# Kernel optimization log

Hardware: AMD Instinct MI355X
Metric: run time of the kernel (lower is better)

The kernel has to match this reference:

```python
import jax, jax.numpy as jnp
import numpy as np

B, L, DIM, H = 2, 2048, 2048, 16
D = DIM // H
EPS = 1e-6
CAP = 50.0
SCALE = D ** -0.5


def _rms_norm(x, w):
    # x: [B,H,L,D], normalize over last dim
    scale = jax.lax.rsqrt(jnp.maximum(jnp.mean(x * x, axis=-1, keepdims=True), EPS))
    return w * x * scale


def _rotate_half(x):
    x1, x2 = jnp.split(x, 2, axis=-1)
    return jnp.concatenate([-x2, x1], axis=-1)


def setup_inputs() -> dict:
    key = jax.random.key(0)
    ks = jax.random.split(key, 6)
    x = jax.random.normal(ks[0], (B, L, DIM), dtype=jnp.float32)
    w_qkv = jax.random.normal(ks[1], (3 * DIM, DIM), dtype=jnp.float32) * (DIM ** -0.5)
    w_out = jax.random.normal(ks[2], (DIM, DIM), dtype=jnp.float32) * (DIM ** -0.5)
    q_norm_w = jnp.ones((D,), dtype=jnp.float32)
    k_norm_w = jnp.ones((D,), dtype=jnp.float32)
    # rope tables [L, D]
    inv_freq = 1.0 / (10000.0 ** (np.arange(0, D, 2, dtype=np.float32) / D))
    t = np.arange(L, dtype=np.float32)
    freqs = np.outer(t, inv_freq)  # [L, D/2]
    emb = np.concatenate([freqs, freqs], axis=-1)  # [L, D]
    cos = jnp.asarray(np.cos(emb), dtype=jnp.float32)
    sin = jnp.asarray(np.sin(emb), dtype=jnp.float32)
    # additive causal mask [1,1,L,L]
    causal = np.triu(np.full((L, L), -1e9, dtype=np.float32), k=1)
    mask = jnp.asarray(causal)[None, None]
    return {"x": x, "w_qkv": w_qkv, "w_out": w_out, "q_norm_w": q_norm_w,
            "k_norm_w": k_norm_w, "cos": cos, "sin": sin, "mask": mask}


def reference(x, w_qkv, w_out, q_norm_w, k_norm_w, cos, sin, mask):
    b, l, _ = x.shape
    qkv = jnp.einsum('bld,ed->ble', x, w_qkv).reshape(b, l, 3, H, D)
    q, k, v = [jnp.transpose(qkv[:, :, i], (0, 2, 1, 3)) for i in range(3)]  # [B,H,L,D]
    q = _rms_norm(q, q_norm_w)
    k = _rms_norm(k, k_norm_w)
    # rope: cos/sin are [L,D] -> [1,1,L,D]
    c = cos[-l:, :][None, None]
    s = sin[-l:, :][None, None]
    q = q * c + _rotate_half(q) * s
    k = k * c + _rotate_half(k) * s
    attn = jnp.einsum('bhqd,bhkd->bhqk', q, k) * SCALE
    attn = jnp.tanh(attn / CAP) * CAP + mask
    probs = jax.nn.softmax(attn, axis=-1)
    o = jnp.einsum('bhqk,bhkd->bhqd', probs, v)
    o = jnp.transpose(o, (0, 2, 1, 3)).reshape(b, l, H * D)
    out = jnp.einsum('bld,ed->ble', o, w_out)
    return (out, (k, v))
```

## Files before the change

kernel.cpp:

```cpp
#include <hip/hip_runtime.h>
#include <hip/hip_bf16.h>
#include <stdint.h>

#define LL 2048
#define DD 128
#define HH 16

typedef float f32x4 __attribute__((ext_vector_type(4)));
typedef float f32x16 __attribute__((ext_vector_type(16)));
typedef float f32x2 __attribute__((ext_vector_type(2)));
typedef short bf16x8 __attribute__((ext_vector_type(8)));
typedef short short4v __attribute__((ext_vector_type(4)));
typedef int int4v __attribute__((ext_vector_type(4)));
typedef float float4v __attribute__((ext_vector_type(4)));

__device__ __forceinline__ float bf2f(short s) {
  union { unsigned u; float f; } v; v.u = ((unsigned)(unsigned short)s) << 16; return v.f;
}
__device__ __forceinline__ short f2bf(float f) {
  union { float f; unsigned u; } v; v.f = f;
  unsigned u = v.u;
  u += 0x7fffu + ((u >> 16) & 1u);
  return (short)(u >> 16);
}
__device__ __forceinline__ unsigned cvtpk(float lo, float hi) {
  unsigned r;
  asm("v_cvt_pk_bf16_f32 %0, %1, %2" : "=v"(r) : "v"(lo), "v"(hi));
  return r;
}

__device__ __forceinline__ void gload_lds16(const void* g, void* lds) {
  __builtin_amdgcn_global_load_lds(
      (__attribute__((address_space(1))) unsigned int*)(void*)(uintptr_t)g,
      (__attribute__((address_space(3))) unsigned int*)lds, 16, 0, 0);
}

__global__ __launch_bounds__(256) void cast_all_kernel(
    const float* __restrict__ x, const float* __restrict__ wqkv,
    const float* __restrict__ wout, short* __restrict__ dst)
{
  long i4 = ((long)blockIdx.x * 256 + threadIdx.x) * 4;
  const float* src; long off;
  if (i4 < 8388608L)        { src = x;    off = i4; }
  else if (i4 < 20971520L)  { src = wqkv; off = i4 - 8388608L; }
  else                      { src = wout; off = i4 - 20971520L; }
  float4v v = *(const float4v*)(src + off);
  short4v o;
  o.x = f2bf(v.x); o.y = f2bf(v.y); o.z = f2bf(v.z); o.w = f2bf(v.w);
  *(short4v*)(dst + i4) = o;
}

#define SCHED __builtin_amdgcn_sched_barrier(0)
#define BARRIER { __builtin_amdgcn_s_barrier(); }

#define STAGE(buf, opx, ptr, rb, ks, t)                                        \
  { _Pragma("unroll") for (int l_ = 0; l_ < 2; ++l_) {                          \
      int ch_ = l_ * 512 + tid;                                                 \
      int row_ = ch_ >> 2, ci_ = ch_ & 3;                                       \
      gload_lds16(ptr + (size_t)(rb + row_) * K + (t) * 64 + (ks) * 32 +        \
                      ((ci_ ^ ((row_ >> 1) & 3)) << 3),                         \
                  &lds[buf][opx][ks][ch_ << 3]);                                \
  } }

#define LDA(buf, mh, ks)                                                       \
  { _Pragma("unroll") for (int mf_ = 0; mf_ < 4; ++mf_) {                       \
      int r_ = wm * 128 + (mh) * 64 + mf_ * 16 + j;                             \
      areg[mf_] = *(const bf16x8*)&lds[buf][0][ks][r_ * 32 + ((g ^ ((j >> 1) & 3)) << 3)]; \
  } }

#define LDB(dst, buf, ks)                                                      \
  { _Pragma("unroll") for (int nf_ = 0; nf_ < 4; ++nf_) {                       \
      int r_ = wn * 64 + nf_ * 16 + j;                                          \
      dst[nf_] = *(const bf16x8*)&lds[buf][1][ks][r_ * 32 + ((g ^ ((j >> 1) & 3)) << 3)]; \
  } }

#define MFMAQ(mh, breg)                                                        \
  { __builtin_amdgcn_s_setprio(1);                                             \
    _Pragma("unroll") for (int mf_ = 0; mf_ < 4; ++mf_)                         \
      _Pragma("unroll") for (int nf_ = 0; nf_ < 4; ++nf_)                       \
        acc[(mh) * 4 + mf_][nf_] = __builtin_amdgcn_mfma_f32_16x16x32_bf16(     \
            areg[mf_], breg[nf_], acc[(mh) * 4 + mf_][nf_], 0, 0, 0);           \
    __builtin_amdgcn_s_setprio(0); }

__global__ __launch_bounds__(512, 2) void gemm256_kernel(
    const short* __restrict__ A, const short* __restrict__ Bm,
    short* __restrict__ C, int M, int N, int K)
{
  __shared__ __align__(16) short lds[2][2][2][8192];
  const int tid = threadIdx.x;
  const int lane = tid & 63;
  const int wid = tid >> 6;
  const int wm = wid >> 2, wn = wid & 3;
  const int g = lane >> 4, j = lane & 15;
  const int m0 = blockIdx.y * 256, n0 = blockIdx.x * 256;
  const int NT = K >> 6;

  f32x4 acc[8][4];
  const f32x4 z = {0.f, 0.f, 0.f, 0.f};
#pragma unroll
  for (int im = 0; im < 8; ++im)
#pragma unroll
    for (int nf = 0; nf < 4; ++nf) acc[im][nf] = z;

  STAGE(0, 1, Bm, n0, 0, 0); STAGE(0, 1, Bm, n0, 1, 0);
  STAGE(0, 0, A,  m0, 0, 0); STAGE(0, 0, A,  m0, 1, 0);
  STAGE(1, 1, Bm, n0, 0, 1); STAGE(1, 1, Bm, n0, 1, 1);
  STAGE(1, 0, A,  m0, 0, 1);
  asm volatile("s_waitcnt vmcnt(6)" ::: "memory");
  __builtin_amdgcn_s_barrier();
  SCHED;

  bf16x8 areg[4], b0r[4], b1r[4];
#pragma unroll 1
  for (int i = 0; i < (NT >> 1) - 1; ++i) {
    int t0 = i * 2;
    LDA(0, 0, 0); LDB(b0r, 0, 0);
    STAGE(1, 0, A, m0, 1, t0 + 1);
    BARRIER; MFMAQ(0, b0r); BARRIER;
    LDA(0, 0, 1); LDB(b1r, 0, 1);
    STAGE(0, 1, Bm, n0, 0, t0 + 2);
    BARRIER; MFMAQ(0, b1r); BARRIER;
    LDA(0, 1, 0);
    STAGE(0, 1, Bm, n0, 1, t0 + 2);
    BARRIER; MFMAQ(1, b0r); BARRIER;
    LDA(0, 1, 1);
    STAGE(0, 0, A, m0, 0, t0 + 2);
    BARRIER; MFMAQ(1, b1r);
    asm volatile("s_waitcnt vmcnt(6)" ::: "memory");
    __builtin_amdgcn_s_barrier(); SCHED;
    LDA(1, 0, 0); LDB(b0r, 1, 0);
    STAGE(0, 0, A, m0, 1, t0 + 2);
    BARRIER; MFMAQ(0, b0r); BARRIER;
    LDA(1, 0, 1); LDB(b1r, 1, 1);
    STAGE(1, 1, Bm, n0, 0, t0 + 3);
    BARRIER; MFMAQ(0, b1r); BARRIER;
    LDA(1, 1, 0);
    STAGE(1, 1, Bm, n0, 1, t0 + 3);
    BARRIER; MFMAQ(1, b0r); BARRIER;
    LDA(1, 1, 1);
    STAGE(1, 0, A, m0, 0, t0 + 3);
    BARRIER; MFMAQ(1, b1r);
    asm volatile("s_waitcnt vmcnt(6)" ::: "memory");
    __builtin_amdgcn_s_barrier(); SCHED;
  }
  {
    LDA(0, 0, 0); LDB(b0r, 0, 0);
    STAGE(1, 0, A, m0, 1, NT - 1);
    BARRIER; MFMAQ(0, b0r); BARRIER;
    LDA(0, 0, 1); LDB(b1r, 0, 1);
    BARRIER; MFMAQ(0, b1r); BARRIER;
    LDA(0, 1, 0);
    BARRIER; MFMAQ(1, b0r); BARRIER;
    LDA(0, 1, 1);
    BARRIER; MFMAQ(1, b1r);
    asm volatile("s_waitcnt vmcnt(0)" ::: "memory");
    __builtin_amdgcn_s_barrier(); SCHED;
    LDA(1, 0, 0); LDB(b0r, 1, 0); MFMAQ(0, b0r);
    LDA(1, 0, 1); LDB(b1r, 1, 1); MFMAQ(0, b1r);
    LDA(1, 1, 0); MFMAQ(1, b0r);
    LDA(1, 1, 1); MFMAQ(1, b1r);
  }
#pragma unroll
  for (int im = 0; im < 8; ++im)
#pragma unroll
    for (int nf = 0; nf < 4; ++nf)
#pragma unroll
      for (int r = 0; r < 4; ++r)
        C[(size_t)(m0 + wm * 128 + im * 16 + g * 4 + r) * N + n0 + wn * 64 + nf * 16 + j] =
            f2bf(acc[im][nf][r]);
}

template <typename OutT>
__global__ __launch_bounds__(256) void gemm_bt_kernel(
    const short* __restrict__ A, const short* __restrict__ Bm,
    OutT* __restrict__ C, int M, int N, int K)
{
  __shared__ __align__(16) short As[128 * 64];
  __shared__ __align__(16) short Bs[128 * 64];
  const int tid = threadIdx.x;
  const int lane = tid & 63;
  const int g = lane >> 4, j = lane & 15;
  const int m0 = blockIdx.y * 128, n0 = blockIdx.x * 128;
  const int wave = tid >> 6;
  const int wm = (wave >> 1) * 64, wn = (wave & 1) * 64;

  f32x4 acc[4][4];
  const f32x4 z = {0.f, 0.f, 0.f, 0.f};
#pragma unroll
  for (int i = 0; i < 4; ++i)
#pragma unroll
    for (int jj = 0; jj < 4; ++jj) acc[i][jj] = z;

  for (int k0 = 0; k0 < K; k0 += 64) {
#pragma unroll
    for (int it = 0; it < 4; ++it) {
      int c = it * 256 + tid;
      int row = c >> 3, ko = (c & 7) << 3;
      gload_lds16(A + (size_t)(m0 + row) * K + k0 + ko, As + c * 8);
    }
#pragma unroll
    for (int it = 0; it < 4; ++it) {
      int c = it * 256 + tid;
      int row = c >> 3, ko = (c & 7) << 3;
      gload_lds16(Bm + (size_t)(n0 + row) * K + k0 + ko, Bs + c * 8);
    }
    __syncthreads();
#pragma unroll
    for (int ks = 0; ks < 2; ++ks) {
      bf16x8 af[4], bfr[4];
#pragma unroll
      for (int i = 0; i < 4; ++i)
        af[i] = *(const bf16x8*)(As + (wm + i * 16 + j) * 64 + ks * 32 + g * 8);
#pragma unroll
      for (int i = 0; i < 4; ++i)
        bfr[i] = *(const bf16x8*)(Bs + (wn + i * 16 + j) * 64 + ks * 32 + g * 8);
#pragma unroll
      for (int i = 0; i < 4; ++i)
#pragma unroll
        for (int jj = 0; jj < 4; ++jj)
          acc[i][jj] = __builtin_amdgcn_mfma_f32_16x16x32_bf16(af[i], bfr[jj], acc[i][jj], 0, 0, 0);
    }
    __syncthreads();
  }
#pragma unroll
  for (int i = 0; i < 4; ++i)
#pragma unroll
    for (int jj = 0; jj < 4; ++jj)
#pragma unroll
      for (int r = 0; r < 4; ++r) {
        int row = m0 + wm + i * 16 + g * 4 + r;
        int col = n0 + wn + jj * 16 + j;
        if constexpr (sizeof(OutT) == 4)
          C[(size_t)row * N + col] = acc[i][jj][r];
        else
          C[(size_t)row * N + col] = f2bf(acc[i][jj][r]);
      }
}

__global__ __launch_bounds__(256) void normrope_kernel(
    const short* __restrict__ qkv, const float* __restrict__ qw,
    const float* __restrict__ kw, const float* __restrict__ cosb,
    const float* __restrict__ sinb, short* __restrict__ qo,
    float* __restrict__ ko, short* __restrict__ kb, float* __restrict__ vo)
{
  int wid = (blockIdx.x * 256 + threadIdx.x) >> 6;
  int lane = threadIdx.x & 63;
  int h = wid & 15;
  int rest = wid >> 4;
  int t = rest % 3;
  int bl = rest / 3;
  int l = bl & (LL - 1);
  int d0 = lane * 2;
  const short* src = qkv + (size_t)bl * 6144 + t * 2048 + h * 128 + d0;
  int raw = *(const int*)src;
  float v0 = bf2f((short)(raw & 0xffff));
  float v1 = bf2f((short)((raw >> 16) & 0xffff));
  size_t oidx = ((size_t)((bl >> 11) * HH + h) * LL + l) * DD + d0;
  if (t == 2) {
    f32x2 vv = {v0, v1};
    *(f32x2*)(vo + oidx) = vv;
    return;
  }
  float ss = v0 * v0 + v1 * v1;
#pragma unroll
  for (int m = 1; m <= 32; m <<= 1) ss += __shfl_xor(ss, m, 64);
  float scale = rsqrtf(fmaxf(ss * (1.0f / 128.0f), 1e-6f));
  const float* w = (t == 0) ? qw : kw;
  float n0 = w[d0] * v0 * scale;
  float n1 = w[d0 + 1] * v1 * scale;
  float c0 = cosb[l * 128 + d0], c1 = cosb[l * 128 + d0 + 1];
  float s0 = sinb[l * 128 + d0], s1 = sinb[l * 128 + d0 + 1];
  float p0 = __shfl_xor(n0, 32, 64);
  float p1 = __shfl_xor(n1, 32, 64);
  float r0 = (lane < 32) ? -p0 : p0;
  float r1 = (lane < 32) ? -p1 : p1;
  float o0 = n0 * c0 + r0 * s0;
  float o1 = n1 * c1 + r1 * s1;
  if (t == 0) {
    const float cu = 0.0017677669529663687f;
    int pk = (int)((unsigned short)f2bf(o0 * cu) |
                   ((unsigned)(unsigned short)f2bf(o1 * cu) << 16));
    *(int*)(qo + oidx) = pk;
  } else {
    f32x2 kk = {o0, o1};
    *(f32x2*)(ko + oidx) = kk;
    int pk = (int)((unsigned short)f2bf(o0) | ((unsigned)(unsigned short)f2bf(o1) << 16));
    *(int*)(kb + oidx) = pk;
  }
}

__global__ __launch_bounds__(256) void transpose_v_kernel(
    const short* __restrict__ qkv, short* __restrict__ vT)
{
  __shared__ __align__(16) short tl[64 * 72];
  int bid = blockIdx.x;
  int dt = bid & 1;
  int lt = (bid >> 1) & 31;
  int bh = bid >> 6;
  int b = bh >> 4, h = bh & 15;
  int tid = threadIdx.x;
#pragma unroll
  for (int it = 0; it < 2; ++it) {
    int c = it * 256 + tid;
    int row = c >> 3, off = (c & 7) << 3;
    int l = lt * 64 + row;
    bf16x8 val = *(const bf16x8*)(qkv + (size_t)(b * LL + l) * 6144 + 4096 + h * 128 + dt * 64 + off);
    *(bf16x8*)(tl + row * 72 + off) = val;
  }
  __syncthreads();
#pragma unroll
  for (int it = 0; it < 2; ++it) {
    int c = it * 256 + tid;
    int dr = c >> 3, lo = (c & 7) << 3;
    bf16x8 o;
#pragma unroll
    for (int i = 0; i < 8; ++i) o[i] = tl[(lo + i) * 72 + dr];
    *(bf16x8*)(vT + ((size_t)bh * DD + dt * 64 + dr) * LL + lt * 64 + lo) = o;
  }
}

#define STAGE_KV(t, buf)                                                       \
  { int k0_ = (t) * 64;                                                        \
    _Pragma("unroll") for (int it_ = 0; it_ < 4; ++it_) {                      \
      int c_ = it_ * 256 + tid;                                                \
      int row_ = c_ >> 4, off_ = (c_ & 15) << 3;                               \
      gload_lds16(kp + (size_t)(k0_ + row_) * DD + (off_ ^ ((row_ & 7) << 3)), \
                  Ks[buf] + c_ * 8);                                           \
    }                                                                          \
    _Pragma("unroll") for (int it_ = 0; it_ < 4; ++it_) {                      \
      int c_ = it_ * 256 + tid;                                                \
      int row_ = c_ >> 3, off_ = (c_ & 7) << 3;                                \
      gload_lds16(vp + (size_t)row_ * LL + k0_ + (off_ ^ ((row_ & 7) << 3)),   \
                  Vs[buf] + c_ * 8);                                           \
    } }

__global__ __launch_bounds__(256, 2) void attn_kernel(
    const short* __restrict__ q, const short* __restrict__ k,
    const short* __restrict__ vT, short* __restrict__ o)
{
  __shared__ __align__(16) short Ks[2][64 * 128];
  __shared__ __align__(16) short Vs[2][128 * 64];
  int bid = blockIdx.x;
  int bh = bid & 31;
  int gq = (bid >> 5) & 7;
  int qt = (bid < 256) ? (15 - gq) : gq;
  int b = bh >> 4;
  int h = bh & 15;
  int tid = threadIdx.x;
  int lane = tid & 63;
  int w = tid >> 6;
  int l31 = lane & 31, lo5 = lane >> 5;
  int q0 = qt * 128;
  int wrow = q0 + w * 32;
  int qg = wrow + l31;

  const short* kp = k + (size_t)bh * LL * DD;
  const short* vp = vT + (size_t)bh * DD * LL;

  bf16x8 qf[8];
#pragma unroll
  for (int ds_ = 0; ds_ < 8; ++ds_)
    qf[ds_] = *(const bf16x8*)(q + ((size_t)bh * LL + qg) * DD + ds_ * 16 + lo5 * 8);

  f32x16 accO[4];
#pragma unroll
  for (int dt = 0; dt < 4; ++dt)
#pragma unroll
    for (int r = 0; r < 16; ++r) accO[dt][r] = 0.f;
  float lsum = 0.f;

  int ktmax = 2 * qt + 1;
  STAGE_KV(0, 0);
  STAGE_KV(1, 1);
  asm volatile("s_waitcnt vmcnt(8)" ::: "memory");
  __builtin_amdgcn_s_barrier();

  for (int kt = 0; kt <= ktmax; ++kt) {
    int k0 = kt * 64;
    const short* Kb = Ks[kt & 1];
    const short* Vb = Vs[kt & 1];

    const bool active = (k0 <= wrow + 31);
    if (active) {
      f32x16 sa[2];
#pragma unroll
      for (int t2 = 0; t2 < 2; ++t2)
#pragma unroll
        for (int r = 0; r < 16; ++r) sa[t2][r] = 0.f;

      __builtin_amdgcn_s_setprio(1);
#pragma unroll
      for (int ds_ = 0; ds_ < 8; ++ds_) {
#pragma unroll
        for (int t2 = 0; t2 < 2; ++t2) {
          int row = t2 * 32 + l31;
          bf16x8 kf = *(const bf16x8*)(Kb + row * 128 +
                          ((ds_ * 16 + lo5 * 8) ^ ((l31 & 7) << 3)));
          sa[t2] = __builtin_amdgcn_mfma_f32_32x32x16_bf16(kf, qf[ds_], sa[t2], 0, 0, 0);
        }
      }
      __builtin_amdgcn_s_setprio(0);

#pragma unroll
      for (int t2 = 0; t2 < 2; ++t2) {
        const bool tmask = (k0 + t2 * 32 + 31) > wrow;
#pragma unroll
        for (int r = 0; r < 16; ++r) {
          float u = sa[t2][r];
          float v2 = u * u;
          float poly = fmaf(v2, fmaf(v2, fmaf(v2, -2.6984127f, 6.6666667f),
                                     -16.666667f), 50.f);
          float p = __expf(fmaf(u, poly, -12.f));
          int kglob = k0 + t2 * 32 + (r & 3) + 8 * (r >> 2) + 4 * lo5;
          if (tmask && (kglob > qg)) p = 0.f;
          lsum += p;
          sa[t2][r] = p;
        }
      }

      __builtin_amdgcn_s_setprio(1);
#pragma unroll
      for (int s = 0; s < 4; ++s) {
        int t2 = s >> 1, RA = 8 * (s & 1), RB = RA + 4;
        unsigned xa0 = cvtpk(sa[t2][RA + 0], sa[t2][RA + 1]);
        unsigned xa1 = cvtpk(sa[t2][RA + 2], sa[t2][RA + 3]);
        unsigned xb0 = cvtpk(sa[t2][RB + 0], sa[t2][RB + 1]);
        unsigned xb1 = cvtpk(sa[t2][RB + 2], sa[t2][RB + 3]);
        unsigned sxa0 = (unsigned)__shfl_xor((int)xa0, 32, 64);
        unsigned sxa1 = (unsigned)__shfl_xor((int)xa1, 32, 64);
        unsigned sxb0 = (unsigned)__shfl_xor((int)xb0, 32, 64);
        unsigned sxb1 = (unsigned)__shfl_xor((int)xb1, 32, 64);
        int4v wv;
        wv.x = (int)(lo5 ? sxb0 : xa0);
        wv.y = (int)(lo5 ? sxb1 : xa1);
        wv.z = (int)(lo5 ? xb0 : sxa0);
        wv.w = (int)(lo5 ? xb1 : sxa1);
        bf16x8 pa = __builtin_bit_cast(bf16x8, wv);
#pragma unroll
        for (int dt = 0; dt < 4; ++dt) {
          int row = dt * 32 + l31;
          bf16x8 vf = *(const bf16x8*)(Vb + row * 64 +
                          ((s * 16 + lo5 * 8) ^ ((l31 & 7) << 3)));
          accO[dt] = __builtin_amdgcn_mfma_f32_32x32x16_bf16(pa, vf, accO[dt], 0, 0, 0);
        }
      }
      __builtin_amdgcn_s_setprio(0);
    }

    __builtin_amdgcn_s_barrier();
    if (kt + 2 <= ktmax) {
      STAGE_KV(kt + 2, kt & 1);
      asm volatile("s_waitcnt vmcnt(8)" ::: "memory");
    } else if (kt + 1 <= ktmax) {
      asm volatile("s_waitcnt vmcnt(0)" ::: "memory");
    }
    __builtin_amdgcn_s_barrier();
  }

  lsum += __shfl_xor(lsum, 32, 64);
  float inv = 1.f / lsum;
#pragma unroll
  for (int r = 0; r < 16; ++r) {
    int qrow = (r & 3) + 8 * (r >> 2) + 4 * lo5;
    float invr = __shfl(inv, qrow, 64);
    size_t obase = ((size_t)b * LL + wrow + qrow) * 2048 + h * 128;
#pragma unroll
    for (int dt = 0; dt < 4; ++dt)
      o[obase + dt * 32 + l31] = f2bf(accO[dt][r] * invr);
  }
}

extern "C" void kernel_launch(void* const* d_in, const int* in_sizes, int n_in,
                              void* d_out, int out_size, void* d_ws, size_t ws_size,
                              hipStream_t stream) {
  const float* x    = (const float*)d_in[0];
  const float* wqkv = (const float*)d_in[1];
  const float* wout = (const float*)d_in[2];
  const float* qw   = (const float*)d_in[3];
  const float* kw   = (const float*)d_in[4];
  const float* cosb = (const float*)d_in[5];
  const float* sinb = (const float*)d_in[6];

  float* out   = (float*)d_out;
  float* k_out = out + 8388608;
  float* v_out = out + 16777216;

  short* ws    = (short*)d_ws;
  short* xb    = ws;
  short* wqkvb = ws + 8388608;
  short* woutb = ws + 20971520;
  short* qkv   = ws + 25165824;
  short* qbuf  = xb;
  short* kbuf  = wqkvb;
  short* vT    = ws + 50331648;
  short* obuf  = qkv;

  cast_all_kernel<<<24576, 256, 0, stream>>>(x, wqkv, wout, ws);
  gemm256_kernel<<<dim3(24, 16), 512, 0, stream>>>(xb, wqkvb, qkv, 4096, 6144, 2048);
  normrope_kernel<<<49152, 256, 0, stream>>>(qkv, qw, kw, cosb, sinb, qbuf, k_out, kbuf, v_out);
  transpose_v_kernel<<<2048, 256, 0, stream>>>(qkv, vT);
  attn_kernel<<<512, 256, 0, stream>>>(qbuf, kbuf, vT, obuf);
  gemm_bt_kernel<float><<<dim3(16, 32), 256, 0, stream>>>(obuf, woutb, out, 4096, 2048, 2048);
}
```

Baseline: 301.4 us.

## Pair causal query tiles per 512-thread block with triple-buffered KV staging

The attention kernel now launches 256 blocks of 512 threads. Each block pairs a long causal query tile (15-p) with a short one (p), so the two tiles share the K/V tiles they load and the work per block is balanced. The K/V shared memory ring grows from two buffers to three, which removes one of the two barriers per iteration. The costs are more LDS per block, only one block per CU by launch bounds, and idle waves in the short-tile half once its rows are done.

```diff
diff --git a/kernel.cpp b/kernel.cpp
--- a/kernel.cpp
+++ b/kernel.cpp
@@ -321,37 +321,36 @@
 
 #define STAGE_KV(t, buf)                                                       \
   { int k0_ = (t) * 64;                                                        \
-    _Pragma("unroll") for (int it_ = 0; it_ < 4; ++it_) {                      \
-      int c_ = it_ * 256 + tid;                                                \
+    _Pragma("unroll") for (int it_ = 0; it_ < 2; ++it_) {                      \
+      int c_ = it_ * 512 + tid;                                                \
       int row_ = c_ >> 4, off_ = (c_ & 15) << 3;                               \
       gload_lds16(kp + (size_t)(k0_ + row_) * DD + (off_ ^ ((row_ & 7) << 3)), \
-                  Ks[buf] + c_ * 8);                                           \
+                  KsA + (buf) * 8192 + c_ * 8);                                \
     }                                                                          \
-    _Pragma("unroll") for (int it_ = 0; it_ < 4; ++it_) {                      \
-      int c_ = it_ * 256 + tid;                                                \
+    _Pragma("unroll") for (int it_ = 0; it_ < 2; ++it_) {                      \
+      int c_ = it_ * 512 + tid;                                                \
       int row_ = c_ >> 3, off_ = (c_ & 7) << 3;                                \
       gload_lds16(vp + (size_t)row_ * LL + k0_ + (off_ ^ ((row_ & 7) << 3)),   \
-                  Vs[buf] + c_ * 8);                                           \
+                  VsA + (buf) * 8192 + c_ * 8);                                \
     } }
 
-__global__ __launch_bounds__(256, 2) void attn_kernel(
+__global__ __launch_bounds__(512, 1) void attn_kernel(
     const short* __restrict__ q, const short* __restrict__ k,
     const short* __restrict__ vT, short* __restrict__ o)
 {
-  __shared__ __align__(16) short Ks[2][64 * 128];
-  __shared__ __align__(16) short Vs[2][128 * 64];
+  __shared__ __align__(16) short KsA[3 * 64 * 128];
+  __shared__ __align__(16) short VsA[3 * 128 * 64];
   int bid = blockIdx.x;
   int bh = bid & 31;
-  int gq = (bid >> 5) & 7;
-  int qt = (bid < 256) ? (15 - gq) : gq;
+  int p = (bid >> 5) & 7;
   int b = bh >> 4;
   int h = bh & 15;
   int tid = threadIdx.x;
   int lane = tid & 63;
   int w = tid >> 6;
   int l31 = lane & 31, lo5 = lane >> 5;
-  int q0 = qt * 128;
-  int wrow = q0 + w * 32;
+  int qt = (w < 4) ? (15 - p) : p;
+  int wrow = qt * 128 + (w & 3) * 32;
   int qg = wrow + l31;
 
   const short* kp = k + (size_t)bh * LL * DD;
@@ -369,16 +368,18 @@
     for (int r = 0; r < 16; ++r) accO[dt][r] = 0.f;
   float lsum = 0.f;
 
-  int ktmax = 2 * qt + 1;
+  const int ktmax = 2 * (15 - p) + 1;
   STAGE_KV(0, 0);
   STAGE_KV(1, 1);
-  asm volatile("s_waitcnt vmcnt(8)" ::: "memory");
+  asm volatile("s_waitcnt vmcnt(4)" ::: "memory");
   __builtin_amdgcn_s_barrier();
 
+  int bufc = 0;
+#pragma unroll 1
   for (int kt = 0; kt <= ktmax; ++kt) {
     int k0 = kt * 64;
-    const short* Kb = Ks[kt & 1];
-    const short* Vb = Vs[kt & 1];
+    const short* Kb = KsA + bufc * 8192;
+    const short* Vb = VsA + bufc * 8192;
 
     const bool active = (k0 <= wrow + 31);
     if (active) {
@@ -410,11 +411,11 @@
           float v2 = u * u;
           float poly = fmaf(v2, fmaf(v2, fmaf(v2, -2.6984127f, 6.6666667f),
                                      -16.666667f), 50.f);
-          float p = __expf(fmaf(u, poly, -12.f));
+          float pe = __expf(fmaf(u, poly, -12.f));
           int kglob = k0 + t2 * 32 + (r & 3) + 8 * (r >> 2) + 4 * lo5;
-          if (tmask && (kglob > qg)) p = 0.f;
-          lsum += p;
-          sa[t2][r] = p;
+          if (tmask && (kglob > qg)) pe = 0.f;
+          lsum += pe;
+          sa[t2][r] = pe;
         }
       }
 
@@ -447,14 +448,16 @@
       __builtin_amdgcn_s_setprio(0);
     }
 
-    __builtin_amdgcn_s_barrier();
     if (kt + 2 <= ktmax) {
-      STAGE_KV(kt + 2, kt & 1);
-      asm volatile("s_waitcnt vmcnt(8)" ::: "memory");
+      int nb = bufc + 2; if (nb >= 3) nb -= 3;
+      STAGE_KV(kt + 2, nb);
+      asm volatile("s_waitcnt vmcnt(4)" ::: "memory");
+      __builtin_amdgcn_s_barrier();
     } else if (kt + 1 <= ktmax) {
       asm volatile("s_waitcnt vmcnt(0)" ::: "memory");
+      __builtin_amdgcn_s_barrier();
     }
-    __builtin_amdgcn_s_barrier();
+    ++bufc; if (bufc == 3) bufc = 0;
   }
 
   lsum += __shfl_xor(lsum, 32, 64);
@@ -499,6 +502,6 @@
   gemm256_kernel<<<dim3(24, 16), 512, 0, stream>>>(xb, wqkvb, qkv, 4096, 6144, 2048);
   normrope_kernel<<<49152, 256, 0, stream>>>(qkv, qw, kw, cosb, sinb, qbuf, k_out, kbuf, v_out);
   transpose_v_kernel<<<2048, 256, 0, stream>>>(qkv, vT);
-  attn_kernel<<<512, 256, 0, stream>>>(qbuf, kbuf, vT, obuf);
+  attn_kernel<<<256, 512, 0, stream>>>(qbuf, kbuf, vT, obuf);
   gemm_bt_kernel<float><<<dim3(16, 32), 256, 0, stream>>>(obuf, woutb, out, 4096, 2048, 2048);
 }
```

After: 297.4 us. Within noise of the previous version (-1.3%).
